# Kernel optimization log

Measured on AMD Instinct MI355X. Metric: run time of the kernel, lower is better.

The kernel has to match this reference:

```python
import jax, jax.numpy as jnp
import numpy as np

N = 50000   # nodes
E = 800000  # random edges (self loops added on top)
C = 64      # in = out channels per head
H = 4       # heads
NEG_SLOPE = 0.2  # PyG GATv2Conv default negative_slope


def setup_inputs() -> dict:
    key = jax.random.key(0)
    ks = jax.random.split(key, 6)
    s = 1.0 / np.sqrt(C)
    x = jax.random.normal(ks[0], (N, C), jnp.float32)
    network_edge = jax.random.randint(ks[1], (2, E), 0, N, dtype=jnp.int64)
    W_l = jax.random.normal(ks[2], (C, H * C), jnp.float32) * s
    b_l = jnp.zeros((H * C,), jnp.float32)
    W_r = jax.random.normal(ks[3], (C, H * C), jnp.float32) * s
    b_r = jnp.zeros((H * C,), jnp.float32)
    att = jax.random.normal(ks[4], (H, C), jnp.float32) * s
    bias = jnp.zeros((C,), jnp.float32)
    return {
        "x": x, "W_l": W_l, "b_l": b_l, "W_r": W_r, "b_r": b_r,
        "att": att, "bias": bias, "network_edge": network_edge,
        "batch_size": 1, "return_attention_weights": 0,
    }


def _gatv2_conv(x, W_l, b_l, W_r, b_r, att, bias, edge_index):
    n = x.shape[0]
    h, c = att.shape
    # add self loops (add_self_loops=True)
    self_idx = jnp.arange(n, dtype=edge_index.dtype)
    src = jnp.concatenate([edge_index[0], self_idx])  # message source j
    dst = jnp.concatenate([edge_index[1], self_idx])  # message target i
    # separate source/target projections (GATv2, share_weights=False)
    xl = (x @ W_l + b_l).reshape(n, h, c)
    xr = (x @ W_r + b_r).reshape(n, h, c)
    # per-edge GATv2 score: a^T LeakyReLU(x_l[j] + x_r[i])
    e = jax.nn.leaky_relu(xl[src] + xr[dst], NEG_SLOPE)  # [Etot,H,C]
    score = jnp.einsum('ehc,hc->eh', e, att)             # [Etot,H]
    # numerically-stable softmax over edges sharing the same target node
    smax = jax.ops.segment_max(score, dst, num_segments=n)  # [n,H]
    ex = jnp.exp(score - smax[dst])
    den = jax.ops.segment_sum(ex, dst, num_segments=n)
    alpha = ex / den[dst]  # dropout=0
    # weighted scatter-aggregate of source features
    out = jax.ops.segment_sum(alpha[:, :, None] * xl[src], dst, num_segments=n)
    out = out.mean(axis=1) + bias  # concat=False -> mean over heads, then bias
    return out, jnp.stack([src, dst]), alpha


def reference(x, W_l, b_l, W_r, b_r, att, bias, network_edge, batch_size,
              return_attention_weights):
    out, ei, alpha = _gatv2_conv(x, W_l, b_l, W_r, b_r, att, bias, network_edge)
    out = out.reshape(batch_size, -1, out.shape[-1])
    if return_attention_weights:
        return out, ei, alpha
    return out
```

## Files before the change

kernel.cpp:

```cpp
#include <hip/hip_runtime.h>

#define TM 16

typedef float v2f __attribute__((ext_vector_type(2)));

__device__ __forceinline__ v2f unpack2(unsigned u) {
    union { unsigned u; float f; } lo, hi;
    lo.u = u << 16;
    hi.u = u & 0xffff0000u;
    v2f r;
    r.x = lo.f;
    r.y = hi.f;
    return r;
}
__device__ __forceinline__ unsigned short f2b(float f) {
    union { float f; unsigned u; } c;
    c.f = f;
    unsigned r = c.u + 0x7fffu + ((c.u >> 16) & 1u);
    return (unsigned short)(r >> 16);
}

__device__ __forceinline__ int edges_are_i64(const unsigned int* raw) {
    int f = 1;
#pragma unroll
    for (int k = 0; k < 16; ++k) f = f && (raw[2 * k + 1] == 0u);
    return f;
}
__device__ __forceinline__ int edge_at(const unsigned int* raw, int f,
                                       size_t idx) {
    return f ? (int)raw[2 * idx] : (int)raw[idx];
}

__global__ __launch_bounds__(256) void k_proj(
    const float* __restrict__ x, const float* __restrict__ Wl,
    const float* __restrict__ bl, const float* __restrict__ Wr,
    const float* __restrict__ br, unsigned short* __restrict__ xl,
    float* __restrict__ xr, int N,
    const unsigned int* __restrict__ eraw, int* __restrict__ deg, int E,
    int Etot) {
    __shared__ float xs[64][TM + 4];
    const int tid = threadIdx.x;
    const int base = blockIdx.x * TM;
    for (int t = tid; t < TM * 64; t += 256) {
        int m = t >> 6, k = t & 63;
        int n = base + m;
        xs[k][m] = (n < N) ? x[(size_t)n * 64 + k] : 0.f;
    }
    __syncthreads();
    const int j = tid;
    v2f accl2[TM / 2], accr2[TM / 2];
    const float blj = bl[j], brj = br[j];
#pragma unroll
    for (int m = 0; m < TM / 2; ++m) {
        accl2[m].x = blj; accl2[m].y = blj;
        accr2[m].x = brj; accr2[m].y = brj;
    }
    for (int k = 0; k < 64; ++k) {
        const float wl = Wl[(size_t)k * 256 + j];
        const float wr = Wr[(size_t)k * 256 + j];
        v2f wl2, wr2;
        wl2.x = wl; wl2.y = wl;
        wr2.x = wr; wr2.y = wr;
        const float4* xrow = (const float4*)(&xs[k][0]);
#pragma unroll
        for (int mm = 0; mm < TM / 4; ++mm) {
            float4 xv = xrow[mm];
            v2f x01, x23;
            x01.x = xv.x; x01.y = xv.y;
            x23.x = xv.z; x23.y = xv.w;
            accl2[2 * mm]     = __builtin_elementwise_fma(x01, wl2, accl2[2 * mm]);
            accl2[2 * mm + 1] = __builtin_elementwise_fma(x23, wl2, accl2[2 * mm + 1]);
            accr2[2 * mm]     = __builtin_elementwise_fma(x01, wr2, accr2[2 * mm]);
            accr2[2 * mm + 1] = __builtin_elementwise_fma(x23, wr2, accr2[2 * mm + 1]);
        }
    }
#pragma unroll
    for (int m = 0; m < TM; ++m) {
        int n = base + m;
        if (n < N) {
            float vl = (m & 1) ? accl2[m >> 1].y : accl2[m >> 1].x;
            float vr = (m & 1) ? accr2[m >> 1].y : accr2[m >> 1].x;
            xl[(size_t)n * 256 + j] = f2b(vl);
            xr[(size_t)n * 256 + j] = vr;
        }
    }
    const int f = edges_are_i64(eraw);
    const int stride = gridDim.x * 256;
    for (int e = blockIdx.x * 256 + tid; e < Etot; e += stride) {
        int d = (e < E) ? edge_at(eraw, f, (size_t)E + e) : (e - E);
        if ((unsigned)d >= (unsigned)N) d = 0;
        atomicAdd(&deg[d], 1);
    }
}

__global__ void k_scanA(const int* __restrict__ deg, int* __restrict__ bsum,
                        int N) {
    __shared__ int s[256];
    int t = threadIdx.x;
    int i = blockIdx.x * 256 + t;
    s[t] = (i < N) ? deg[i] : 0;
    __syncthreads();
    for (int d = 128; d > 0; d >>= 1) {
        if (t < d) s[t] += s[t + d];
        __syncthreads();
    }
    if (t == 0) bsum[blockIdx.x] = s[0];
}

__global__ void k_scanC(const int* __restrict__ deg,
                        const int* __restrict__ bsum,
                        int* __restrict__ row_start, int* __restrict__ cursor,
                        int Etot, int N) {
    __shared__ int s[256];
    __shared__ int off_s;
    const int t = threadIdx.x;
    s[t] = (t < blockIdx.x) ? bsum[t] : 0;
    __syncthreads();
    for (int d = 128; d > 0; d >>= 1) {
        if (t < d) s[t] += s[t + d];
        __syncthreads();
    }
    if (t == 0) off_s = s[0];
    __syncthreads();
    const int offset = off_s;
    __syncthreads();
    const int i = blockIdx.x * 256 + t;
    const int v = (i < N) ? deg[i] : 0;
    s[t] = v;
    __syncthreads();
    for (int d = 1; d < 256; d <<= 1) {
        int add = (t >= d) ? s[t - d] : 0;
        __syncthreads();
        s[t] += add;
        __syncthreads();
    }
    if (i < N) {
        int rs = s[t] - v + offset;
        row_start[i] = rs;
        cursor[i] = rs;
    }
    if (blockIdx.x == gridDim.x - 1 && t == 0) row_start[N] = Etot;
}

__global__ void k_scatter(const unsigned int* __restrict__ raw,
                          int* __restrict__ cursor, int* __restrict__ csr_src,
                          int E, int Etot, int N) {
    int e = blockIdx.x * 256 + threadIdx.x;
    if (e >= Etot) return;
    int f = edges_are_i64(raw);
    int s, d;
    if (e < E) {
        s = edge_at(raw, f, (size_t)e);
        d = edge_at(raw, f, (size_t)E + e);
    } else {
        s = d = e - E;
    }
    if ((unsigned)s >= (unsigned)N) s = 0;
    if ((unsigned)d >= (unsigned)N) d = 0;
    int slot = atomicAdd(&cursor[d], 1);
    if ((unsigned)slot < (unsigned)Etot) csr_src[slot] = s;
}

__global__ __launch_bounds__(256) void k_aggregate(
    const unsigned short* __restrict__ xl, const float* __restrict__ xr,
    const float* __restrict__ att, const float* __restrict__ bias,
    const int* __restrict__ row_start, const int* __restrict__ csr_src,
    float* __restrict__ out, int N) {
    const int wave = threadIdx.x >> 6;
    const int lane = threadIdx.x & 63;
    const int i = blockIdx.x * 4 + wave;
    if (i >= N) return;
    const int half = lane >> 5;
    const int sl = lane & 31;
    const int co = sl * 8;

    v2f xrv[4], av[4];
    {
        const float4 x0 = *(const float4*)(xr + (size_t)i * 256 + co);
        const float4 x1 = *(const float4*)(xr + (size_t)i * 256 + co + 4);
        xrv[0].x = x0.x; xrv[0].y = x0.y;
        xrv[1].x = x0.z; xrv[1].y = x0.w;
        xrv[2].x = x1.x; xrv[2].y = x1.y;
        xrv[3].x = x1.z; xrv[3].y = x1.w;
        const float4 a0 = *(const float4*)(att + co);
        const float4 a1 = *(const float4*)(att + co + 4);
        av[0].x = a0.x; av[0].y = a0.y;
        av[1].x = a0.z; av[1].y = a0.w;
        av[2].x = a1.x; av[2].y = a1.y;
        av[3].x = a1.z; av[3].y = a1.w;
    }
    v2f accv[4];
#pragma unroll
    for (int p = 0; p < 4; ++p) { accv[p].x = 0.f; accv[p].y = 0.f; }
    float den = 0.f;
    const int beg = row_start[i];
    const int end = row_start[i + 1];
    const int last = end - 1;
    const unsigned short* xlo = xl + co;

    constexpr int D = 3;
    uint4 cur[D];
    int sidx[D];
#pragma unroll
    for (int d = 0; d < D; ++d) {
        int s = csr_src[min(beg + 2 * d + half, last)];
        cur[d] = *(const uint4*)(xlo + (size_t)s * 256);
    }
#pragma unroll
    for (int d = 0; d < D; ++d)
        sidx[d] = csr_src[min(beg + 2 * D + 2 * d + half, last)];

    for (int e = beg; e < end; e += 2 * D) {
#pragma unroll
        for (int d = 0; d < D; ++d) {
            const uint4 cu = cur[d];
            cur[d] = *(const uint4*)(xlo + (size_t)sidx[d] * 256);
            sidx[d] = csr_src[min(e + 4 * D + 2 * d + half, last)];

            v2f c0 = unpack2(cu.x), c1 = unpack2(cu.y);
            v2f c2 = unpack2(cu.z), c3 = unpack2(cu.w);
            v2f v0 = c0 + xrv[0], v1 = c1 + xrv[1];
            v2f v2 = c2 + xrv[2], v3 = c3 + xrv[3];
            v0 = __builtin_elementwise_max(v0, v0 * 0.2f);
            v1 = __builtin_elementwise_max(v1, v1 * 0.2f);
            v2 = __builtin_elementwise_max(v2, v2 * 0.2f);
            v3 = __builtin_elementwise_max(v3, v3 * 0.2f);
            v2f t2a = av[0] * v0;
            v2f t2b = av[1] * v1;
            t2a = __builtin_elementwise_fma(av[2], v2, t2a);
            t2b = __builtin_elementwise_fma(av[3], v3, t2b);
            t2a += t2b;
            float t = t2a.x + t2a.y;
            t += __shfl_xor(t, 1);
            t += __shfl_xor(t, 2);
            t += __shfl_xor(t, 4);
            float w = __expf(fminf(t, 60.f));
            w = (e + 2 * d + half <= last) ? w : 0.f;
            den += w;
            v2f w2;
            w2.x = w; w2.y = w;
            accv[0] = __builtin_elementwise_fma(w2, c0, accv[0]);
            accv[1] = __builtin_elementwise_fma(w2, c1, accv[1]);
            accv[2] = __builtin_elementwise_fma(w2, c2, accv[2]);
            accv[3] = __builtin_elementwise_fma(w2, c3, accv[3]);
        }
    }
    den += __shfl_xor(den, 32);
    float r[8];
    r[0] = accv[0].x; r[1] = accv[0].y; r[2] = accv[1].x; r[3] = accv[1].y;
    r[4] = accv[2].x; r[5] = accv[2].y; r[6] = accv[3].x; r[7] = accv[3].y;
#pragma unroll
    for (int j = 0; j < 8; ++j) r[j] += __shfl_xor(r[j], 32);
    const float inv = 1.f / den;
#pragma unroll
    for (int j = 0; j < 8; ++j) r[j] *= inv;
#pragma unroll
    for (int j = 0; j < 8; ++j) {
        r[j] += __shfl_xor(r[j], 8);
        r[j] += __shfl_xor(r[j], 16);
    }
    if (lane < 8) {
        const float4 b0 = *(const float4*)(bias + lane * 8);
        const float4 b1 = *(const float4*)(bias + lane * 8 + 4);
        *(float4*)(out + (size_t)i * 64 + lane * 8) =
            make_float4(b0.x + 0.25f * r[0], b0.y + 0.25f * r[1],
                        b0.z + 0.25f * r[2], b0.w + 0.25f * r[3]);
        *(float4*)(out + (size_t)i * 64 + lane * 8 + 4) =
            make_float4(b1.x + 0.25f * r[4], b1.y + 0.25f * r[5],
                        b1.z + 0.25f * r[6], b1.w + 0.25f * r[7]);
    }
}

extern "C" void kernel_launch(void* const* d_in, const int* in_sizes, int n_in,
                              void* d_out, int out_size, void* d_ws,
                              size_t ws_size, hipStream_t stream) {
    const float* x    = (const float*)d_in[0];
    const float* Wl   = (const float*)d_in[1];
    const float* bl   = (const float*)d_in[2];
    const float* Wr   = (const float*)d_in[3];
    const float* br   = (const float*)d_in[4];
    const float* att  = (const float*)d_in[5];
    const float* bias = (const float*)d_in[6];
    const unsigned int* edges_raw = (const unsigned int*)d_in[7];

    const int N = in_sizes[0] / 64;
    const int E = in_sizes[7] / 2;
    const int Etot = E + N;

    char* p = (char*)d_ws;
    size_t off = 0;
    auto carve = [&](size_t bytes) -> char* {
        char* r = p + off;
        off = (off + bytes + 255) & ~(size_t)255;
        return r;
    };
    unsigned short* xl = (unsigned short*)carve((size_t)N * 256 * 2);
    float* xr      = (float*)carve((size_t)N * 256 * 4);
    int* csr_src   = (int*)carve((size_t)Etot * 4);
    int* row_start = (int*)carve((size_t)(N + 1) * 4);
    int* deg       = (int*)carve((size_t)N * 4);
    int* cursor    = (int*)carve((size_t)N * 4);
    int* bsum      = (int*)carve(1024 * 4);

    hipMemsetAsync(deg, 0, (size_t)N * 4, stream);

    k_proj<<<(N + TM - 1) / TM, 256, 0, stream>>>(x, Wl, bl, Wr, br, xl, xr, N,
                                                  edges_raw, deg, E, Etot);
    const int NB = (N + 255) / 256;
    k_scanA<<<NB, 256, 0, stream>>>(deg, bsum, N);
    k_scanC<<<NB, 256, 0, stream>>>(deg, bsum, row_start, cursor, Etot, N);
    k_scatter<<<(Etot + 255) / 256, 256, 0, stream>>>(edges_raw, cursor,
                                                      csr_src, E, Etot, N);
    k_aggregate<<<(N + 3) / 4, 256, 0, stream>>>(xl, xr, att, bias, row_start,
                                                 csr_src, (float*)d_out, N);
}
```

Measured before the change: 262.6 us.

## Retile projection kernel to two columns per thread and deepen aggregate prefetch

```diff
diff --git a/kernel.cpp b/kernel.cpp
--- a/kernel.cpp
+++ b/kernel.cpp
@@ -38,50 +38,66 @@
     float* __restrict__ xr, int N,
     const unsigned int* __restrict__ eraw, int* __restrict__ deg, int E,
     int Etot) {
-    __shared__ float xs[64][TM + 4];
+    __shared__ __align__(16) float xs[2][64][TM + 4];
     const int tid = threadIdx.x;
-    const int base = blockIdx.x * TM;
-    for (int t = tid; t < TM * 64; t += 256) {
+    const int base = blockIdx.x * (2 * TM);
+    for (int t = tid; t < 2 * TM * 64; t += 256) {
         int m = t >> 6, k = t & 63;
         int n = base + m;
-        xs[k][m] = (n < N) ? x[(size_t)n * 64 + k] : 0.f;
-    }
-    __syncthreads();
-    const int j = tid;
-    v2f accl2[TM / 2], accr2[TM / 2];
-    const float blj = bl[j], brj = br[j];
+        xs[m >> 4][k][m & 15] = (n < N) ? x[(size_t)n * 64 + k] : 0.f;
+    }
+    __syncthreads();
+    const int c = tid & 127;
+    const int rt = tid >> 7;
+    const int j0 = 2 * c;
+    v2f al0[TM / 2], al1[TM / 2], ar0[TM / 2], ar1[TM / 2];
+    const float bl0 = bl[j0], bl1 = bl[j0 + 1];
+    const float br0 = br[j0], br1 = br[j0 + 1];
 #pragma unroll
     for (int m = 0; m < TM / 2; ++m) {
-        accl2[m].x = blj; accl2[m].y = blj;
-        accr2[m].x = brj; accr2[m].y = brj;
+        al0[m].x = bl0; al0[m].y = bl0;
+        al1[m].x = bl1; al1[m].y = bl1;
+        ar0[m].x = br0; ar0[m].y = br0;
+        ar1[m].x = br1; ar1[m].y = br1;
     }
     for (int k = 0; k < 64; ++k) {
-        const float wl = Wl[(size_t)k * 256 + j];
-        const float wr = Wr[(size_t)k * 256 + j];
-        v2f wl2, wr2;
-        wl2.x = wl; wl2.y = wl;
-        wr2.x = wr; wr2.y = wr;
-        const float4* xrow = (const float4*)(&xs[k][0]);
+        const float2 wl = ((const float2*)(Wl + (size_t)k * 256))[c];
+        const float2 wr = ((const float2*)(Wr + (size_t)k * 256))[c];
+        v2f wl0, wl1, wr0, wr1;
+        wl0.x = wl.x; wl0.y = wl.x;
+        wl1.x = wl.y; wl1.y = wl.y;
+        wr0.x = wr.x; wr0.y = wr.x;
+        wr1.x = wr.y; wr1.y = wr.y;
+        const float4* xrow = (const float4*)(&xs[rt][k][0]);
 #pragma unroll
         for (int mm = 0; mm < TM / 4; ++mm) {
             float4 xv = xrow[mm];
             v2f x01, x23;
             x01.x = xv.x; x01.y = xv.y;
             x23.x = xv.z; x23.y = xv.w;
-            accl2[2 * mm]     = __builtin_elementwise_fma(x01, wl2, accl2[2 * mm]);
-            accl2[2 * mm + 1] = __builtin_elementwise_fma(x23, wl2, accl2[2 * mm + 1]);
-            accr2[2 * mm]     = __builtin_elementwise_fma(x01, wr2, accr2[2 * mm]);
-            accr2[2 * mm + 1] = __builtin_elementwise_fma(x23, wr2, accr2[2 * mm + 1]);
+            al0[2 * mm]     = __builtin_elementwise_fma(x01, wl0, al0[2 * mm]);
+            al0[2 * mm + 1] = __builtin_elementwise_fma(x23, wl0, al0[2 * mm + 1]);
+            al1[2 * mm]     = __builtin_elementwise_fma(x01, wl1, al1[2 * mm]);
+            al1[2 * mm + 1] = __builtin_elementwise_fma(x23, wl1, al1[2 * mm + 1]);
+            ar0[2 * mm]     = __builtin_elementwise_fma(x01, wr0, ar0[2 * mm]);
+            ar0[2 * mm + 1] = __builtin_elementwise_fma(x23, wr0, ar0[2 * mm + 1]);
+            ar1[2 * mm]     = __builtin_elementwise_fma(x01, wr1, ar1[2 * mm]);
+            ar1[2 * mm + 1] = __builtin_elementwise_fma(x23, wr1, ar1[2 * mm + 1]);
         }
     }
 #pragma unroll
     for (int m = 0; m < TM; ++m) {
-        int n = base + m;
+        int n = base + rt * TM + m;
         if (n < N) {
-            float vl = (m & 1) ? accl2[m >> 1].y : accl2[m >> 1].x;
-            float vr = (m & 1) ? accr2[m >> 1].y : accr2[m >> 1].x;
-            xl[(size_t)n * 256 + j] = f2b(vl);
-            xr[(size_t)n * 256 + j] = vr;
+            float vl0 = (m & 1) ? al0[m >> 1].y : al0[m >> 1].x;
+            float vl1 = (m & 1) ? al1[m >> 1].y : al1[m >> 1].x;
+            float vr0 = (m & 1) ? ar0[m >> 1].y : ar0[m >> 1].x;
+            float vr1 = (m & 1) ? ar1[m >> 1].y : ar1[m >> 1].x;
+            unsigned pk = (unsigned)f2b(vl0) | ((unsigned)f2b(vl1) << 16);
+            *(unsigned*)(xl + (size_t)n * 256 + j0) = pk;
+            float2 vr;
+            vr.x = vr0; vr.y = vr1;
+            *(float2*)(xr + (size_t)n * 256 + j0) = vr;
         }
     }
     const int f = edges_are_i64(eraw);
@@ -198,7 +214,7 @@
     const int last = end - 1;
     const unsigned short* xlo = xl + co;
 
-    constexpr int D = 3;
+    constexpr int D = 4;
     uint4 cur[D];
     int sidx[D];
 #pragma unroll
@@ -304,8 +320,8 @@
 
     hipMemsetAsync(deg, 0, (size_t)N * 4, stream);
 
-    k_proj<<<(N + TM - 1) / TM, 256, 0, stream>>>(x, Wl, bl, Wr, br, xl, xr, N,
-                                                  edges_raw, deg, E, Etot);
+    k_proj<<<(N + 2 * TM - 1) / (2 * TM), 256, 0, stream>>>(
+        x, Wl, bl, Wr, br, xl, xr, N, edges_raw, deg, E, Etot);
     const int NB = (N + 255) / 256;
     k_scanA<<<NB, 256, 0, stream>>>(deg, bsum, N);
     k_scanC<<<NB, 256, 0, stream>>>(deg, bsum, row_start, cursor, Etot, N);
```

Result: slower. 269.1 us (+2.5%).
